# Optimization experiments

Measured on AMD Instinct MI355X. Metric: run time of the kernel, lower is better.

## Reference

```python
import jax, jax.numpy as jnp
import numpy as np

D_IN = 768
D_OUT = 768
NUM_HEADS = 12
HEAD_DIM = D_OUT // NUM_HEADS


def setup_inputs() -> dict:
    key = jax.random.key(0)
    ks = jax.random.split(key, 6)
    s = 0.02
    x = jax.random.normal(ks[0], (4, 1024, D_IN), dtype=jnp.float32)
    # torch Linear weights are [out_features, in_features]
    Wq = jax.random.normal(ks[1], (D_OUT, D_IN), dtype=jnp.float32) * s
    Wk = jax.random.normal(ks[2], (D_OUT, D_IN), dtype=jnp.float32) * s
    Wv = jax.random.normal(ks[3], (D_OUT, D_IN), dtype=jnp.float32) * s
    Wo = jax.random.normal(ks[4], (D_OUT, D_OUT), dtype=jnp.float32) * s
    bo = jax.random.normal(ks[5], (D_OUT,), dtype=jnp.float32) * s
    return {"x": x, "Wq": Wq, "Wk": Wk, "Wv": Wv, "Wo": Wo, "bo": bo}


def reference(x, Wq, Wk, Wv, Wo, bo):
    B, T, _ = x.shape
    H, Dh = NUM_HEADS, HEAD_DIM
    # QKV projections (no bias), reshape to [B, H, T, Dh]
    q = (x @ Wq.T).reshape(B, T, H, Dh).transpose(0, 2, 1, 3)
    k = (x @ Wk.T).reshape(B, T, H, Dh).transpose(0, 2, 1, 3)
    v = (x @ Wv.T).reshape(B, T, H, Dh).transpose(0, 2, 1, 3)
    # Scores [B, H, T, T]. NOTE: original torch code's masked_fill and dropout
    # are not in-place / not assigned, so neither affects the output.
    scores = jnp.einsum("bhqd,bhkd->bhqk", q, k)
    attn = jax.nn.softmax(scores / np.sqrt(Dh).astype(np.float32), axis=-1)
    ctx = jnp.einsum("bhqk,bhkd->bhqd", attn, v)
    ctx = ctx.transpose(0, 2, 1, 3).reshape(B, T, H * Dh)
    return ctx @ Wo.T + bo
```

## Files before the change

kernel.cpp:

```cpp
#include <hip/hip_runtime.h>

typedef _Float16 half8 __attribute__((ext_vector_type(8)));
typedef float f32x4 __attribute__((ext_vector_type(4)));
typedef unsigned short u16;

#define NHEAD 12
#define DHEAD 64
#define DM    768
#define TSEQ  1024
#define LOG2E 1.44269504f

static constexpr size_t OFF_XH  = 0;
static constexpr size_t OFF_WQH = 3145728;
static constexpr size_t OFF_WKH = 3735552;
static constexpr size_t OFF_WVH = 4325376;
static constexpr size_t OFF_WOH = 4915200;
static constexpr size_t OFF_Q   = 5505024;
static constexpr size_t OFF_K   = 8650752;
static constexpr size_t OFF_VT  = 11796480;
static constexpr size_t OFF_CTX = 0;
static constexpr size_t OFF_OP  = 14942208;
static constexpr size_t OFF_ML_BYTES = 42467328;
static constexpr size_t WS_NEED_SPLITK = 43253760;

typedef const __attribute__((address_space(1))) void* gas_ptr;
typedef __attribute__((address_space(3))) void* las_ptr;
__device__ __forceinline__ void gload16(const _Float16* g, _Float16* l) {
    __builtin_amdgcn_global_load_lds((gas_ptr)g, (las_ptr)l, 16, 0, 0);
}

template <int CTRL>
__device__ __forceinline__ float dpp_rotf(float x) {
    int r = __builtin_amdgcn_update_dpp(0, __builtin_bit_cast(int, x), CTRL, 0xF, 0xF, true);
    return __builtin_bit_cast(float, r);
}
__device__ __forceinline__ float row16_max(float x) {
    x = fmaxf(x, dpp_rotf<0x121>(x));
    x = fmaxf(x, dpp_rotf<0x122>(x));
    x = fmaxf(x, dpp_rotf<0x124>(x));
    x = fmaxf(x, dpp_rotf<0x128>(x));
    return x;
}
__device__ __forceinline__ float row16_add(float x) {
    x = x + dpp_rotf<0x121>(x);
    x = x + dpp_rotf<0x122>(x);
    x = x + dpp_rotf<0x124>(x);
    x = x + dpp_rotf<0x128>(x);
    return x;
}

__global__ void cvt_kernel(const float* __restrict__ x, const float* __restrict__ wq,
                           const float* __restrict__ wk, const float* __restrict__ wv,
                           const float* __restrict__ wo, _Float16* __restrict__ ws) {
    int i = (blockIdx.x * 256 + threadIdx.x) * 8;
    const float* src;
    if (i < 3145728)      src = x  + i;
    else if (i < 3735552) src = wq + (i - 3145728);
    else if (i < 4325376) src = wk + (i - 3735552);
    else if (i < 4915200) src = wv + (i - 4325376);
    else                  src = wo + (i - 4915200);
    float4 v0 = *(const float4*)(src);
    float4 v1 = *(const float4*)(src + 4);
    half8 o;
    o[0] = (_Float16)v0.x; o[1] = (_Float16)v0.y;
    o[2] = (_Float16)v0.z; o[3] = (_Float16)v0.w;
    o[4] = (_Float16)v1.x; o[5] = (_Float16)v1.y;
    o[6] = (_Float16)v1.z; o[7] = (_Float16)v1.w;
    *(half8*)(ws + i) = o;
}

__global__ __launch_bounds__(256) void qkv_kernel(_Float16* __restrict__ ws) {
    __shared__ __align__(16) _Float16 ldsA[128 * 64];
    __shared__ __align__(16) _Float16 ldsB[128 * 64];

    const int z = blockIdx.z;
    const _Float16* __restrict__ xh = ws + OFF_XH;
    const _Float16* __restrict__ w  = ws + (z == 0 ? OFF_WQH : z == 1 ? OFF_WKH : OFF_WVH);
    _Float16* __restrict__ outp     = ws + (z == 0 ? OFF_Q   : z == 1 ? OFF_K   : OFF_VT);

    const int tid  = threadIdx.x;
    const int lane = tid & 63;
    const int wid  = tid >> 6;
    const int quad = lane >> 4, l15 = lane & 15;
    const int wm = (wid & 1) * 64, wn = (wid >> 1) * 64;

    int mb, nb;
    const _Float16 *gA, *gB;
    if (z < 2) {
        mb = blockIdx.x * 128;
        nb = blockIdx.y * 128;
        gA = xh + (size_t)mb * DM;
        gB = w  + (size_t)nb * DM;
    } else {
        mb = blockIdx.y * 128;
        nb = blockIdx.x * 128;
        gA = w  + (size_t)mb * DM;
        gB = xh + (size_t)nb * DM;
    }

    const int srow = tid >> 3;
    const int scol = (tid & 7) * 8;

    f32x4 acc[4][4] = {};
    for (int k0 = 0; k0 < DM; k0 += 64) {
#pragma unroll
        for (int c = 0; c < 4; c++) {
            gload16(gA + (size_t)(c * 32 + srow) * DM + scol + k0, ldsA + c * 2048 + wid * 512);
            gload16(gB + (size_t)(c * 32 + srow) * DM + scol + k0, ldsB + c * 2048 + wid * 512);
        }
        __syncthreads();

#pragma unroll
        for (int ks = 0; ks < 2; ks++) {
            half8 a[4], b[4];
#pragma unroll
            for (int t = 0; t < 4; t++) {
                a[t] = *(const half8*)(ldsA + (wm + t * 16 + l15) * 64 + ks * 32 + quad * 8);
                b[t] = *(const half8*)(ldsB + (wn + t * 16 + l15) * 64 + ks * 32 + quad * 8);
            }
#pragma unroll
            for (int mt = 0; mt < 4; mt++)
#pragma unroll
                for (int nt = 0; nt < 4; nt++)
                    acc[mt][nt] = __builtin_amdgcn_mfma_f32_16x16x32_f16(a[mt], b[nt], acc[mt][nt], 0, 0, 0);
        }
        __syncthreads();
    }

#pragma unroll
    for (int mt = 0; mt < 4; mt++)
#pragma unroll
        for (int nt = 0; nt < 4; nt++)
#pragma unroll
            for (int r = 0; r < 4; r++) {
                int m = mb + wm + mt * 16 + quad * 4 + r;
                int n = nb + wn + nt * 16 + l15;
                size_t idx;
                if (z < 2) {
                    int bb = m >> 10, tt = m & 1023;
                    int h = n >> 6, d = n & 63;
                    idx = ((size_t)(bb * NHEAD + h) * TSEQ + tt) * DHEAD + d;
                } else {
                    int h = m >> 6, d = m & 63;
                    int bb = n >> 10, tt = n & 1023;
                    idx = ((size_t)(bb * NHEAD + h) * DHEAD + d) * TSEQ + tt;
                }
                outp[idx] = (_Float16)acc[mt][nt][r];
            }
}

template <int NZ>
__device__ __forceinline__ void attn_body(_Float16* __restrict__ ws) {
    __shared__ __align__(16) _Float16 ldsK[64 * 64];
    __shared__ __align__(16) _Float16 ldsV[64 * 64];
    __shared__ __align__(16) _Float16 ldsP[4][16 * 72];

    const int tid  = threadIdx.x;
    const int lane = tid & 63;
    const int wid  = tid >> 6;
    const int quad = lane >> 4, l15 = lane & 15;
    const int bh = blockIdx.y;
    const int z  = (NZ > 1) ? blockIdx.z : 0;
    const int q0 = blockIdx.x * 64 + wid * 16;
    const int kbeg = z * (TSEQ / NZ), kend = kbeg + TSEQ / NZ;

    const _Float16* __restrict__ Q  = ws + OFF_Q  + (size_t)bh * TSEQ * DHEAD;
    const _Float16* __restrict__ K  = ws + OFF_K  + (size_t)bh * TSEQ * DHEAD;
    const _Float16* __restrict__ VT = ws + OFF_VT + (size_t)bh * DHEAD * TSEQ;
    _Float16* pbase = ldsP[wid];

    const int srow0 = tid >> 3, sc0 = tid & 7;
    const int ldsOff0 = srow0 * 64 + ((sc0 ^ (srow0 & 7)) * 8);
    const int ldsOff1 = (srow0 + 32) * 64 + ((sc0 ^ (srow0 & 7)) * 8);

    half8 qf[2];
#pragma unroll
    for (int ks = 0; ks < 2; ks++) {
        qf[ks] = *(const half8*)(Q + (size_t)(q0 + l15) * DHEAD + ks * 32 + quad * 8);
        qf[ks] = qf[ks] * (_Float16)0.125f;
    }

    float mrun[4], lrun[4];
    f32x4 oacc[4] = {};
#pragma unroll
    for (int r = 0; r < 4; r++) { mrun[r] = -1e30f; lrun[r] = 0.f; }

    uint4 ka, kb, va, vb;
    ka = *(const uint4*)(K + kbeg * DHEAD + tid * 8);
    kb = *(const uint4*)(K + kbeg * DHEAD + 2048 + tid * 8);
    va = *(const uint4*)(VT + (size_t)srow0 * TSEQ + kbeg + sc0 * 8);
    vb = *(const uint4*)(VT + (size_t)(srow0 + 32) * TSEQ + kbeg + sc0 * 8);

    for (int kt = kbeg; kt < kend; kt += 64) {
        *(uint4*)(ldsK + ldsOff0) = ka;
        *(uint4*)(ldsK + ldsOff1) = kb;
        *(uint4*)(ldsV + ldsOff0) = va;
        *(uint4*)(ldsV + ldsOff1) = vb;
        __syncthreads();

        if (kt + 64 < kend) {
            ka = *(const uint4*)(K + (kt + 64) * DHEAD + tid * 8);
            kb = *(const uint4*)(K + (kt + 64) * DHEAD + 2048 + tid * 8);
            va = *(const uint4*)(VT + (size_t)srow0 * TSEQ + kt + 64 + sc0 * 8);
            vb = *(const uint4*)(VT + (size_t)(srow0 + 32) * TSEQ + kt + 64 + sc0 * 8);
        }

        half8 kf[4][2];
#pragma unroll
        for (int n = 0; n < 4; n++)
#pragma unroll
            for (int ks = 0; ks < 2; ks++) {
                int row = n * 16 + l15;
                int phys = (ks * 4 + quad) ^ (row & 7);
                kf[n][ks] = *(const half8*)(ldsK + row * 64 + phys * 8);
            }

        f32x4 s[4] = {};
#pragma unroll
        for (int n = 0; n < 4; n++)
#pragma unroll
            for (int ks = 0; ks < 2; ks++)
                s[n] = __builtin_amdgcn_mfma_f32_16x16x32_f16(qf[ks], kf[n][ks], s[n], 0, 0, 0);

        float tm[4];
#pragma unroll
        for (int r = 0; r < 4; r++) {
            float t = fmaxf(fmaxf(s[0][r], s[1][r]), fmaxf(s[2][r], s[3][r]));
            tm[r] = row16_max(t);
        }
        float need = fmaxf(fmaxf(tm[0] - mrun[0], tm[1] - mrun[1]),
                           fmaxf(tm[2] - mrun[2], tm[3] - mrun[3]));
        if (!__all(need <= 4.0f)) {
#pragma unroll
            for (int r = 0; r < 4; r++) {
                float mnew = fmaxf(mrun[r], tm[r]);
                float alpha = __builtin_amdgcn_exp2f((mrun[r] - mnew) * LOG2E);
                mrun[r] = mnew;
                lrun[r] *= alpha;
#pragma unroll
                for (int dn = 0; dn < 4; dn++) oacc[dn][r] *= alpha;
            }
        }
#pragma unroll
        for (int r = 0; r < 4; r++) {
            float mL = mrun[r] * LOG2E;
            float ts = 0.f;
#pragma unroll
            for (int n = 0; n < 4; n++) {
                float e = __builtin_amdgcn_exp2f(__builtin_fmaf(s[n][r], LOG2E, -mL));
                s[n][r] = e;
                ts += e;
            }
            ts = row16_add(ts);
            lrun[r] += ts;
        }

#pragma unroll
        for (int n = 0; n < 4; n++)
#pragma unroll
            for (int r = 0; r < 4; r++)
                pbase[(quad * 4 + r) * 72 + n * 16 + l15] = (_Float16)s[n][r];

        half8 vf[4][2];
#pragma unroll
        for (int dn = 0; dn < 4; dn++)
#pragma unroll
            for (int ks = 0; ks < 2; ks++) {
                int row = dn * 16 + l15;
                int phys = (ks * 4 + quad) ^ (row & 7);
                vf[dn][ks] = *(const half8*)(ldsV + row * 64 + phys * 8);
            }

        half8 pf[2];
#pragma unroll
        for (int ks = 0; ks < 2; ks++)
            pf[ks] = *(const half8*)(pbase + l15 * 72 + ks * 32 + quad * 8);

#pragma unroll
        for (int dn = 0; dn < 4; dn++)
#pragma unroll
            for (int ks = 0; ks < 2; ks++)
                oacc[dn] = __builtin_amdgcn_mfma_f32_16x16x32_f16(pf[ks], vf[dn][ks], oacc[dn], 0, 0, 0);

        __syncthreads();
    }

    if (NZ == 1) {
        _Float16* __restrict__ ctx = ws + OFF_CTX;
        const int b_ = bh / NHEAD, h = bh % NHEAD;
#pragma unroll
        for (int dn = 0; dn < 4; dn++)
#pragma unroll
            for (int r = 0; r < 4; r++) {
                int t_ = q0 + quad * 4 + r;
                int col = h * DHEAD + dn * 16 + l15;
                float v = oacc[dn][r] / lrun[r];
                ctx[((size_t)(b_ * TSEQ + t_)) * DM + col] = (_Float16)v;
            }
    } else {
        _Float16* __restrict__ op = ws + OFF_OP;
        float* __restrict__ ml = (float*)((char*)ws + OFF_ML_BYTES);
        const size_t rowbase = (size_t)z * 48 * TSEQ + (size_t)bh * TSEQ + q0;
#pragma unroll
        for (int dn = 0; dn < 4; dn++)
#pragma unroll
            for (int r = 0; r < 4; r++) {
                size_t row = rowbase + quad * 4 + r;
                op[row * 64 + dn * 16 + l15] = (_Float16)oacc[dn][r];
            }
        if (l15 == 0) {
#pragma unroll
            for (int r = 0; r < 4; r++) {
                size_t row = rowbase + quad * 4 + r;
                ml[row * 2]     = mrun[r];
                ml[row * 2 + 1] = lrun[r];
            }
        }
    }
}

__global__ __launch_bounds__(256, 3) void attn_kernel(_Float16* __restrict__ ws) {
    attn_body<1>(ws);
}
__global__ __launch_bounds__(256, 4) void attn_splitk_kernel(_Float16* __restrict__ ws) {
    attn_body<2>(ws);
}

__global__ __launch_bounds__(256) void combine_kernel(_Float16* __restrict__ ws) {
    const _Float16* __restrict__ op = ws + OFF_OP;
    const float* __restrict__ ml = (const float*)((const char*)ws + OFF_ML_BYTES);
    _Float16* __restrict__ ctx = ws + OFF_CTX;

    int g = blockIdx.x * 256 + threadIdx.x;
    int row = g >> 3, chunk = g & 7;
    int bh = row >> 10, q = row & 1023;
    int b_ = bh / NHEAD, h = bh % NHEAD;

    float m0 = ml[(size_t)row * 2], l0 = ml[(size_t)row * 2 + 1];
    float m1 = ml[(size_t)(49152 + row) * 2], l1 = ml[(size_t)(49152 + row) * 2 + 1];
    float M = fmaxf(m0, m1);
    float w0 = __builtin_amdgcn_exp2f((m0 - M) * LOG2E);
    float w1 = __builtin_amdgcn_exp2f((m1 - M) * LOG2E);
    float inv_l = 1.0f / (w0 * l0 + w1 * l1);

    half8 o0 = *(const half8*)(op + (size_t)row * 64 + chunk * 8);
    half8 o1 = *(const half8*)(op + (size_t)(49152 + row) * 64 + chunk * 8);
    half8 o;
#pragma unroll
    for (int j = 0; j < 8; j++)
        o[j] = (_Float16)(((float)o0[j] * w0 + (float)o1[j] * w1) * inv_l);
    *(half8*)(ctx + ((size_t)(b_ * TSEQ + q)) * DM + h * DHEAD + chunk * 8) = o;
}

__global__ __launch_bounds__(256) void proj_kernel(const _Float16* __restrict__ ws,
                                                   const float* __restrict__ bo,
                                                   float* __restrict__ out) {
    __shared__ __align__(16) _Float16 ldsA[64 * 64];
    __shared__ __align__(16) _Float16 ldsB[64 * 64];

    const _Float16* __restrict__ gA = ws + OFF_CTX + (size_t)blockIdx.x * 64 * DM;
    const _Float16* __restrict__ gB = ws + OFF_WOH + (size_t)blockIdx.y * 64 * DM;

    const int tid  = threadIdx.x;
    const int lane = tid & 63;
    const int wid  = tid >> 6;
    const int quad = lane >> 4, l15 = lane & 15;
    const int wm = (wid & 1) * 32, wn = (wid >> 1) * 32;

    const int srow = tid >> 3;
    const int scol = (tid & 7) * 8;

    f32x4 acc[2][2] = {};
    for (int k0 = 0; k0 < DM; k0 += 64) {
#pragma unroll
        for (int c = 0; c < 2; c++) {
            gload16(gA + (size_t)(c * 32 + srow) * DM + scol + k0, ldsA + c * 2048 + wid * 512);
            gload16(gB + (size_t)(c * 32 + srow) * DM + scol + k0, ldsB + c * 2048 + wid * 512);
        }
        __syncthreads();

#pragma unroll
        for (int ks = 0; ks < 2; ks++) {
            half8 a[2], b[2];
#pragma unroll
            for (int t = 0; t < 2; t++) {
                a[t] = *(const half8*)(ldsA + (wm + t * 16 + l15) * 64 + ks * 32 + quad * 8);
                b[t] = *(const half8*)(ldsB + (wn + t * 16 + l15) * 64 + ks * 32 + quad * 8);
            }
#pragma unroll
            for (int mt = 0; mt < 2; mt++)
#pragma unroll
                for (int nt = 0; nt < 2; nt++)
                    acc[mt][nt] = __builtin_amdgcn_mfma_f32_16x16x32_f16(a[mt], b[nt], acc[mt][nt], 0, 0, 0);
        }
        __syncthreads();
    }

    const int mb = blockIdx.x * 64, nb = blockIdx.y * 64;
#pragma unroll
    for (int mt = 0; mt < 2; mt++)
#pragma unroll
        for (int nt = 0; nt < 2; nt++)
#pragma unroll
            for (int r = 0; r < 4; r++) {
                int m = mb + wm + mt * 16 + quad * 4 + r;
                int n = nb + wn + nt * 16 + l15;
                out[(size_t)m * DM + n] = acc[mt][nt][r] + bo[n];
            }
}

extern "C" void kernel_launch(void* const* d_in, const int* in_sizes, int n_in,
                              void* d_out, int out_size, void* d_ws, size_t ws_size,
                              hipStream_t stream) {
    const float* x  = (const float*)d_in[0];
    const float* wq = (const float*)d_in[1];
    const float* wk = (const float*)d_in[2];
    const float* wv = (const float*)d_in[3];
    const float* wo = (const float*)d_in[4];
    const float* bo = (const float*)d_in[5];
    _Float16* ws = (_Float16*)d_ws;
    float* out = (float*)d_out;

    cvt_kernel<<<dim3(2688, 1, 1), 256, 0, stream>>>(x, wq, wk, wv, wo, ws);
    qkv_kernel<<<dim3(32, 6, 3), 256, 0, stream>>>(ws);
    if (ws_size >= WS_NEED_SPLITK) {
        attn_splitk_kernel<<<dim3(16, 48, 2), 256, 0, stream>>>(ws);
        combine_kernel<<<dim3(1536, 1, 1), 256, 0, stream>>>(ws);
    } else {
        attn_kernel<<<dim3(16, 48, 1), 256, 0, stream>>>(ws);
    }
    proj_kernel<<<dim3(64, 12, 1), 256, 0, stream>>>(ws, bo, out);
}
```

Before: 162.2 us.

## Double-buffer LDS tiles and XOR-swizzle layout in QKV and projection GEMMs

The QKV and output-projection GEMMs now use two LDS buffers, so the global-to-LDS load of the next K tile is issued before computing on the current one. Staged columns are XOR-swizzled by row, and the fragment reads apply the matching swizzle to reduce LDS bank conflicts. Double buffering doubles LDS use per block, which may lower occupancy (the QKV kernel goes to 64KB). The attention kernel is unchanged.

```diff
diff --git a/kernel.cpp b/kernel.cpp
--- a/kernel.cpp
+++ b/kernel.cpp
@@ -70,8 +70,8 @@
 }
 
 __global__ __launch_bounds__(256) void qkv_kernel(_Float16* __restrict__ ws) {
-    __shared__ __align__(16) _Float16 ldsA[128 * 64];
-    __shared__ __align__(16) _Float16 ldsB[128 * 64];
+    __shared__ __align__(16) _Float16 ldsA[2][128 * 64];
+    __shared__ __align__(16) _Float16 ldsB[2][128 * 64];
 
     const int z = blockIdx.z;
     const _Float16* __restrict__ xh = ws + OFF_XH;
@@ -99,24 +99,32 @@
     }
 
     const int srow = tid >> 3;
-    const int scol = (tid & 7) * 8;
+    const int scol = (((tid & 7) ^ (srow & 7)) * 8);
+
+    auto stage = [&](int buf, int k0) {
+#pragma unroll
+        for (int c = 0; c < 4; c++) {
+            gload16(gA + (size_t)(c * 32 + srow) * DM + scol + k0, &ldsA[buf][c * 2048 + wid * 512]);
+            gload16(gB + (size_t)(c * 32 + srow) * DM + scol + k0, &ldsB[buf][c * 2048 + wid * 512]);
+        }
+    };
 
     f32x4 acc[4][4] = {};
+    stage(0, 0);
+    __syncthreads();
+    int cur = 0;
     for (int k0 = 0; k0 < DM; k0 += 64) {
-#pragma unroll
-        for (int c = 0; c < 4; c++) {
-            gload16(gA + (size_t)(c * 32 + srow) * DM + scol + k0, ldsA + c * 2048 + wid * 512);
-            gload16(gB + (size_t)(c * 32 + srow) * DM + scol + k0, ldsB + c * 2048 + wid * 512);
-        }
-        __syncthreads();
-
+        if (k0 + 64 < DM) stage(cur ^ 1, k0 + 64);
+        const _Float16* lA = ldsA[cur];
+        const _Float16* lB = ldsB[cur];
 #pragma unroll
         for (int ks = 0; ks < 2; ks++) {
             half8 a[4], b[4];
 #pragma unroll
             for (int t = 0; t < 4; t++) {
-                a[t] = *(const half8*)(ldsA + (wm + t * 16 + l15) * 64 + ks * 32 + quad * 8);
-                b[t] = *(const half8*)(ldsB + (wn + t * 16 + l15) * 64 + ks * 32 + quad * 8);
+                const int phys = (((ks * 4 + quad) ^ (l15 & 7)) * 8);
+                a[t] = *(const half8*)(lA + (wm + t * 16 + l15) * 64 + phys);
+                b[t] = *(const half8*)(lB + (wn + t * 16 + l15) * 64 + phys);
             }
 #pragma unroll
             for (int mt = 0; mt < 4; mt++)
@@ -125,6 +133,7 @@
                     acc[mt][nt] = __builtin_amdgcn_mfma_f32_16x16x32_f16(a[mt], b[nt], acc[mt][nt], 0, 0, 0);
         }
         __syncthreads();
+        cur ^= 1;
     }
 
 #pragma unroll
@@ -355,8 +364,8 @@
 __global__ __launch_bounds__(256) void proj_kernel(const _Float16* __restrict__ ws,
                                                    const float* __restrict__ bo,
                                                    float* __restrict__ out) {
-    __shared__ __align__(16) _Float16 ldsA[64 * 64];
-    __shared__ __align__(16) _Float16 ldsB[64 * 64];
+    __shared__ __align__(16) _Float16 ldsA[2][64 * 64];
+    __shared__ __align__(16) _Float16 ldsB[2][64 * 64];
 
     const _Float16* __restrict__ gA = ws + OFF_CTX + (size_t)blockIdx.x * 64 * DM;
     const _Float16* __restrict__ gB = ws + OFF_WOH + (size_t)blockIdx.y * 64 * DM;
@@ -368,24 +377,32 @@
     const int wm = (wid & 1) * 32, wn = (wid >> 1) * 32;
 
     const int srow = tid >> 3;
-    const int scol = (tid & 7) * 8;
+    const int scol = (((tid & 7) ^ (srow & 7)) * 8);
+
+    auto stage = [&](int buf, int k0) {
+#pragma unroll
+        for (int c = 0; c < 2; c++) {
+            gload16(gA + (size_t)(c * 32 + srow) * DM + scol + k0, &ldsA[buf][c * 2048 + wid * 512]);
+            gload16(gB + (size_t)(c * 32 + srow) * DM + scol + k0, &ldsB[buf][c * 2048 + wid * 512]);
+        }
+    };
 
     f32x4 acc[2][2] = {};
+    stage(0, 0);
+    __syncthreads();
+    int cur = 0;
     for (int k0 = 0; k0 < DM; k0 += 64) {
-#pragma unroll
-        for (int c = 0; c < 2; c++) {
-            gload16(gA + (size_t)(c * 32 + srow) * DM + scol + k0, ldsA + c * 2048 + wid * 512);
-            gload16(gB + (size_t)(c * 32 + srow) * DM + scol + k0, ldsB + c * 2048 + wid * 512);
-        }
-        __syncthreads();
-
+        if (k0 + 64 < DM) stage(cur ^ 1, k0 + 64);
+        const _Float16* lA = ldsA[cur];
+        const _Float16* lB = ldsB[cur];
 #pragma unroll
         for (int ks = 0; ks < 2; ks++) {
             half8 a[2], b[2];
 #pragma unroll
             for (int t = 0; t < 2; t++) {
-                a[t] = *(const half8*)(ldsA + (wm + t * 16 + l15) * 64 + ks * 32 + quad * 8);
-                b[t] = *(const half8*)(ldsB + (wn + t * 16 + l15) * 64 + ks * 32 + quad * 8);
+                const int phys = (((ks * 4 + quad) ^ (l15 & 7)) * 8);
+                a[t] = *(const half8*)(lA + (wm + t * 16 + l15) * 64 + phys);
+                b[t] = *(const half8*)(lB + (wn + t * 16 + l15) * 64 + phys);
             }
 #pragma unroll
             for (int mt = 0; mt < 2; mt++)
@@ -394,6 +411,7 @@
                     acc[mt][nt] = __builtin_amdgcn_mfma_f32_16x16x32_f16(a[mt], b[nt], acc[mt][nt], 0, 0, 0);
         }
         __syncthreads();
+        cur ^= 1;
     }
 
     const int mb = blockIdx.x * 64, nb = blockIdx.y * 64;
```

Result: faster. 151.5 us (-6.6%).
